# Performance work log

Hardware: AMD Instinct MI355X
Metric: run time of the kernel (lower is better)

The kernel has to match this reference:

```python
import jax, jax.numpy as jnp
import numpy as np
from jax import lax

K = 3  # kernel_size


def _leaky(x):
    return jnp.where(x >= 0, x, 0.1 * x)


def _conv3x3(x, w, b):
    # x: (B,C,H,W), w: (O,C,3,3)
    out = lax.conv_general_dilated(x, w, (1, 1), [(1, 1), (1, 1)],
                                   dimension_numbers=('NCHW', 'OIHW', 'NCHW'))
    return out + b[None, :, None, None]


def _da_conv(x, d, kw1, kw2, cw, cb, ca1, ca2):
    # per-sample dynamic depthwise conv + 1x1 conv + channel attention
    b, c, h, w = x.shape
    p = (K - 1) // 2
    # predicted per-(sample,channel) KxK kernels: (b, c*K*K) -> (b*c, 1, K, K)
    kern = (_leaky(d @ kw1.T) @ kw2.T).reshape(b * c, 1, K, K)
    out = lax.conv_general_dilated(x.reshape(1, b * c, h, w), kern, (1, 1),
                                   [(p, p), (p, p)], feature_group_count=b * c,
                                   dimension_numbers=('NCHW', 'OIHW', 'NCHW'))
    out = _leaky(out).reshape(b, c, h, w)
    # 1x1 conv with bias
    out = jnp.einsum('bchw,oc->bohw', out, cw) + cb[None, :, None, None]
    # CA layer: sigmoid(W2 @ leaky(W1 @ d)) per sample
    att = jax.nn.sigmoid(_leaky(d @ ca1.T) @ ca2.T)  # (b, c_out)
    return out + x * att[:, :, None, None]


def _forward(x, d,
             da1_kw1, da1_kw2, da1_cw, da1_cb, da1_ca1, da1_ca2,
             da2_kw1, da2_kw2, da2_cw, da2_cb, da2_ca1, da2_ca2,
             conv1_w, conv1_b, conv2_w, conv2_b, conv3_w, conv3_b,
             add_w1, add_w2):
    out = _leaky(_da_conv(x, d, da1_kw1, da1_kw2, da1_cw, da1_cb, da1_ca1, da1_ca2))
    out = _leaky(_conv3x3(out, conv1_w, conv1_b))
    # additive map: (b, 1024) -> (b,1,32,32) -> nearest-upsample to (H,W)
    add = (_leaky(d @ add_w1.T) @ add_w2.T).reshape(-1, 1, 32, 32)
    H = out.shape[-1]
    idx = jnp.arange(H) * 32 // H  # PyTorch 'nearest' index rule
    add = add[:, :, idx[:, None], idx[None, :]]
    out = out + add
    out = _conv3x3(out, conv2_w, conv2_b)
    out = _leaky(_da_conv(out, d, da2_kw1, da2_kw2, da2_cw, da2_cb, da2_ca1, da2_ca2))
    return _conv3x3(out, conv3_w, conv3_b) + x


def setup_inputs() -> dict:
    B, C, H, W = 8, 64, 192, 192
    RED = 8
    key = jax.random.key(0)
    ks = jax.random.split(key, 24)
    n = lambda k, shape, s=0.05: jax.random.normal(k, shape, jnp.float32) * s
    inp = {
        'x': jax.random.normal(ks[0], (B, C, H, W), jnp.float32),
        'd': jax.random.normal(ks[1], (B, C), jnp.float32),
    }
    for i, pfx in enumerate(['da1', 'da2']):
        base = 2 + i * 6
        inp[f'{pfx}_kw1'] = n(ks[base + 0], (64, 64))
        inp[f'{pfx}_kw2'] = n(ks[base + 1], (C * K * K, 64))
        inp[f'{pfx}_cw'] = n(ks[base + 2], (C, C))   # 1x1 conv weight (O,I)
        inp[f'{pfx}_cb'] = n(ks[base + 3], (C,))
        inp[f'{pfx}_ca1'] = n(ks[base + 4], (C // RED, 64))
        inp[f'{pfx}_ca2'] = n(ks[base + 5], (C, C // RED))
    for i, pfx in enumerate(['conv1', 'conv2', 'conv3']):
        inp[f'{pfx}_w'] = n(ks[14 + 2 * i], (C, C, K, K))
        inp[f'{pfx}_b'] = n(ks[15 + 2 * i], (C,))
    inp['add_w1'] = n(ks[20], (64, 64))
    inp['add_w2'] = n(ks[21], (32 * 32, 64))
    return inp


def reference(x, d,
              da1_kw1, da1_kw2, da1_cw, da1_cb, da1_ca1, da1_ca2,
              da2_kw1, da2_kw2, da2_cw, da2_cb, da2_ca1, da2_ca2,
              conv1_w, conv1_b, conv2_w, conv2_b, conv3_w, conv3_b,
              add_w1, add_w2):
    return _forward(x, d,
                    da1_kw1, da1_kw2, da1_cw, da1_cb, da1_ca1, da1_ca2,
                    da2_kw1, da2_kw2, da2_cw, da2_cb, da2_ca1, da2_ca2,
                    conv1_w, conv1_b, conv2_w, conv2_b, conv3_w, conv3_b,
                    add_w1, add_w2)
```

## Files before the change

kernel.cpp:

```cpp
#include <hip/hip_runtime.h>
#include <math.h>

#define B_ 8
#define C_ 64
#define H_ 192
#define W_ 192
#define HW_ (H_*W_)

typedef __attribute__((ext_vector_type(8))) short bf16x8;
typedef __attribute__((ext_vector_type(4))) float f32x4;
typedef __attribute__((ext_vector_type(4))) unsigned short u16x4;
typedef __attribute__((ext_vector_type(8))) unsigned short u16x8;
typedef __attribute__((ext_vector_type(4))) unsigned int u32x4;

__device__ __forceinline__ float lk(float v){ return v >= 0.f ? v : 0.1f*v; }
__device__ __forceinline__ float bf2f(unsigned short h){ return __uint_as_float(((unsigned)h)<<16); }
__device__ __forceinline__ unsigned short f2bf(float f){
    unsigned u = __float_as_uint(f);
    return (unsigned short)((u + 0x7fffu + ((u>>16)&1u)) >> 16);
}
__device__ __forceinline__ f32x4 mfma16(bf16x8 a, bf16x8 b, f32x4 c){
    return __builtin_amdgcn_mfma_f32_16x16x32_bf16(a, b, c, 0, 0, 0);
}

__device__ __forceinline__ void xcd_decomp(int L, int& b, int& h0, int& w0){
    b = L & 7;
    int t = L >> 3;
    h0 = (t / 12) * 16;
    w0 = (t % 12) * 16;
}

#define XS_ELEMS 22528

__global__ __launch_bounds__(256) void k_small(
    const float* __restrict__ d,
    const float* __restrict__ kw1a, const float* __restrict__ kw2a,
    const float* __restrict__ ca1a, const float* __restrict__ ca2a,
    const float* __restrict__ kw1b, const float* __restrict__ kw2b,
    const float* __restrict__ ca1b, const float* __restrict__ ca2b,
    const float* __restrict__ aw1,  const float* __restrict__ aw2,
    float* __restrict__ kern1, float* __restrict__ att1,
    float* __restrict__ kern2, float* __restrict__ att2,
    float* __restrict__ addm)
{
    int b = blockIdx.x, tid = threadIdx.x;
    __shared__ float sd[64], sv[64], su[8];
    if (tid < 64) sd[tid] = d[b*64 + tid];
    __syncthreads();
    if (tid < 64){ float s=0.f; for(int k=0;k<64;k++) s += sd[k]*kw1a[tid*64+k]; sv[tid]=lk(s); }
    if (tid >= 64 && tid < 72){ int r=tid-64; float s=0.f; for(int k=0;k<64;k++) s += sd[k]*ca1a[r*64+k]; su[r]=lk(s); }
    __syncthreads();
    for (int i=tid;i<576;i+=256){ float s=0.f; for(int j=0;j<64;j++) s += sv[j]*kw2a[i*64+j]; kern1[b*576+i]=s; }
    if (tid < 64){ float s=0.f; for(int r=0;r<8;r++) s += su[r]*ca2a[tid*8+r]; att1[b*64+tid]=1.f/(1.f+expf(-s)); }
    __syncthreads();
    if (tid < 64){ float s=0.f; for(int k=0;k<64;k++) s += sd[k]*kw1b[tid*64+k]; sv[tid]=lk(s); }
    if (tid >= 64 && tid < 72){ int r=tid-64; float s=0.f; for(int k=0;k<64;k++) s += sd[k]*ca1b[r*64+k]; su[r]=lk(s); }
    __syncthreads();
    for (int i=tid;i<576;i+=256){ float s=0.f; for(int j=0;j<64;j++) s += sv[j]*kw2b[i*64+j]; kern2[b*576+i]=s; }
    if (tid < 64){ float s=0.f; for(int r=0;r<8;r++) s += su[r]*ca2b[tid*8+r]; att2[b*64+tid]=1.f/(1.f+expf(-s)); }
    __syncthreads();
    if (tid < 64){ float s=0.f; for(int k=0;k<64;k++) s += sd[k]*aw1[tid*64+k]; sv[tid]=lk(s); }
    __syncthreads();
    for (int i=tid;i<1024;i+=256){ float s=0.f; for(int j=0;j<64;j++) s += sv[j]*aw2[i*64+j]; addm[b*1024+i]=s; }
}

__global__ __launch_bounds__(256) void k_prep(
    const float* __restrict__ w1, const float* __restrict__ w2, const float* __restrict__ w3,
    const float* __restrict__ cw1, const float* __restrict__ cw2,
    unsigned short* __restrict__ wA1, unsigned short* __restrict__ wA2, unsigned short* __restrict__ wA3,
    unsigned short* __restrict__ cwA1, unsigned short* __restrict__ cwA2,
    unsigned short* __restrict__ zp)
{
    int blk = blockIdx.x;
    if (blk < 192){
        const float* w = (blk < 64) ? w1 : (blk < 128) ? w2 : w3;
        unsigned short* wA = (blk < 64) ? wA1 : (blk < 128) ? wA2 : wA3;
        int oc = blk & 63;
        for (int i = threadIdx.x; i < 576; i += 256){
            int t = i >> 6, ic = i & 63;
            wA[oc*576 + i] = f2bf(w[oc*576 + ic*9 + t]);
        }
    } else {
        int i = (blk - 192)*256 + threadIdx.x;
        if (i < 4096) cwA1[i] = f2bf(cw1[i]);
        else          cwA2[i-4096] = f2bf(cw2[i-4096]);
        if (blk == 223 && threadIdx.x < 32) zp[threadIdx.x] = 0;
    }
}

__global__ __launch_bounds__(256) void k_xprep(const float* __restrict__ xf, unsigned short* __restrict__ xb){
    int L = blockIdx.x;
    int b = L & 7, px0 = (L >> 3)*256;
    int tid = threadIdx.x;
    __shared__ unsigned short ts[256*64];
    int q = tid >> 5, p = tid & 31;
    #pragma unroll 1
    for (int j=0; j<8; j++){
        int px = p + 32*j;
        u16x8 o;
        #pragma unroll
        for (int i=0; i<8; i++)
            o[i] = f2bf(xf[((size_t)(b*64 + q*8 + i))*HW_ + px0 + px]);
        *(u16x8*)&ts[px*64 + ((q ^ (px&7))*8)] = o;
    }
    __syncthreads();
    int k = tid & 7, pg = tid >> 3;
    #pragma unroll 1
    for (int j=0; j<8; j++){
        int px = pg + 32*j;
        u32x4 v = *(const u32x4*)&ts[px*64 + ((k ^ (px&7))*8)];
        *(u32x4*)&xb[((size_t)(b*HW_) + px0 + px)*64 + k*8] = v;
    }
}

__device__ __forceinline__ void stage_gl(const unsigned short* __restrict__ in,
                                         unsigned short* xs,
                                         const unsigned short* __restrict__ zp,
                                         int b, int h0, int w0, int wv, int lane)
{
    #pragma unroll
    for (int i=0; i<11; i++){
        int e = i*256 + wv*64 + lane;
        int pix = e >> 3;
        int j = (e & 7) ^ (pix & 7);
        int r = pix/18, col = pix - r*18;
        int gh = h0 - 1 + r, gw = w0 - 1 + col;
        const unsigned short* src = (gh >= 0 && gh < H_ && gw >= 0 && gw < W_)
            ? &in[((size_t)(b*HW_ + gh*W_ + gw))*64 + j*8] : zp;
        __builtin_amdgcn_global_load_lds(
            (const __attribute__((address_space(1))) void*)src,
            (__attribute__((address_space(3))) void*)&xs[(size_t)(i*256 + wv*64)*8],
            16, 0, 0);
    }
}

__device__ __forceinline__ void conv_main(const unsigned short* xs,
                                          const unsigned short* __restrict__ wbase,
                                          bf16x8 afr[2][2],
                                          int n, int g, int rowbase, f32x4 acc[2][8])
{
    #pragma unroll 1
    for (int t=0; t<9; t++){
        bf16x8 nxt[2][2];
        if (t < 8){
            #pragma unroll
            for (int mf=0; mf<2; mf++)
                #pragma unroll
                for (int kf=0; kf<2; kf++)
                    nxt[mf][kf] = *(const bf16x8*)(wbase + mf*(16*576) + (t+1)*64 + kf*32);
        }
        int dy = t/3, dx = t - dy*3;
        #pragma unroll
        for (int r=0; r<8; r++){
            int pix = (rowbase + r + dy)*18 + (n + dx);
            int sw = pix & 7;
            #pragma unroll
            for (int kf=0; kf<2; kf++){
                bf16x8 bfr = *(const bf16x8*)&xs[pix*64 + (((kf*4+g) ^ sw)*8)];
                acc[0][r] = mfma16(afr[0][kf], bfr, acc[0][r]);
                acc[1][r] = mfma16(afr[1][kf], bfr, acc[1][r]);
            }
        }
        if (t < 8){
            #pragma unroll
            for (int mf=0; mf<2; mf++)
                #pragma unroll
                for (int kf=0; kf<2; kf++) afr[mf][kf] = nxt[mf][kf];
        }
    }
}

template<int MODE>
__global__ __launch_bounds__(256) void k_conv(
    const unsigned short* __restrict__ in,
    const unsigned short* __restrict__ wA,
    const float* __restrict__ bias,
    const float* __restrict__ addm,
    const unsigned short* __restrict__ zp,
    unsigned short* __restrict__ outb)
{
    int b, h0, w0; xcd_decomp(blockIdx.x, b, h0, w0);
    int tid = threadIdx.x;
    __shared__ unsigned short xs[XS_ELEMS];

    int lane = tid & 63, wv = tid >> 6;
    int n = lane & 15, g = lane >> 4;
    int ochalf = (wv & 1)*32, rowbase = (wv >> 1)*8;

    stage_gl(in, xs, zp, b, h0, w0, wv, lane);

    const unsigned short* wbase = wA + (size_t)(ochalf + n)*576 + g*8;
    bf16x8 afr[2][2];
    #pragma unroll
    for (int mf=0; mf<2; mf++)
        #pragma unroll
        for (int kf=0; kf<2; kf++)
            afr[mf][kf] = *(const bf16x8*)(wbase + mf*(16*576) + kf*32);

    __syncthreads();

    f32x4 acc[2][8];
    f32x4 zz = {0.f,0.f,0.f,0.f};
    #pragma unroll
    for (int mf=0; mf<2; mf++)
        #pragma unroll
        for (int r=0; r<8; r++) acc[mf][r] = zz;

    conv_main(xs, wbase, afr, n, g, rowbase, acc);

    #pragma unroll
    for (int r=0; r<8; r++){
        int h = h0 + rowbase + r, w = w0 + n;
        float addv = 0.f;
        if (MODE == 0) addv = addm[b*1024 + (h/6)*32 + (w/6)];
        #pragma unroll
        for (int mf=0; mf<2; mf++){
            int oc0 = ochalf + mf*16 + g*4;
            f32x4 v = acc[mf][r];
            f32x4 b4 = *(const f32x4*)&bias[oc0];
            u16x4 o;
            #pragma unroll
            for (int j=0;j<4;j++){
                float val = v[j] + b4[j];
                if (MODE == 0) val = lk(val) + addv;
                o[j] = f2bf(val);
            }
            *(u16x4*)&outb[((size_t)(b*HW_ + h*W_ + w))*64 + oc0] = o;
        }
    }
}

__global__ __launch_bounds__(256) void kc3(
    const unsigned short* __restrict__ in,
    const unsigned short* __restrict__ wA,
    const float* __restrict__ bias,
    const unsigned short* __restrict__ xresb,
    const unsigned short* __restrict__ zp,
    float* __restrict__ outf)
{
    int b, h0, w0; xcd_decomp(blockIdx.x, b, h0, w0);
    int tid = threadIdx.x;
    __shared__ unsigned short xs[XS_ELEMS];

    int lane = tid & 63, wv = tid >> 6;
    int n = lane & 15, g = lane >> 4;
    int ochalf = (wv & 1)*32, rowbase = (wv >> 1)*8;

    stage_gl(in, xs, zp, b, h0, w0, wv, lane);

    const unsigned short* wbase = wA + (size_t)(ochalf + n)*576 + g*8;
    bf16x8 afr[2][2];
    #pragma unroll
    for (int mf=0; mf<2; mf++)
        #pragma unroll
        for (int kf=0; kf<2; kf++)
            afr[mf][kf] = *(const bf16x8*)(wbase + mf*(16*576) + kf*32);

    __syncthreads();

    f32x4 acc[2][8];
    f32x4 zz = {0.f,0.f,0.f,0.f};
    #pragma unroll
    for (int mf=0; mf<2; mf++)
        #pragma unroll
        for (int r=0; r<8; r++) acc[mf][r] = zz;

    conv_main(xs, wbase, afr, n, g, rowbase, acc);

    __syncthreads();
    unsigned short* ys = xs;

    #pragma unroll
    for (int mf=0; mf<2; mf++){
        int oc0 = ochalf + mf*16 + g*4;
        int sw = ((oc0 >> 2) & 3) << 2;
        f32x4 b4 = *(const f32x4*)&bias[oc0];
        #pragma unroll
        for (int r=0; r<8; r++){
            int h = h0 + rowbase + r, w = w0 + n;
            int px = (rowbase + r)*16 + n;
            u16x4 xr = *(const u16x4*)&xresb[((size_t)(b*HW_ + h*W_ + w))*64 + oc0];
            f32x4 v = acc[mf][r];
            #pragma unroll
            for (int j=0; j<4; j++)
                ys[(oc0 + j)*256 + (px ^ sw)] = f2bf(v[j] + b4[j] + bf2f(xr[j]));
        }
    }
    __syncthreads();

    int q = lane & 3, rr = lane >> 2;
    #pragma unroll 1
    for (int pass=0; pass<16; pass++){
        int oc = wv + pass*4;
        int sw = ((oc >> 2) & 3) << 2;
        int px = (rr*16 + q*4) ^ sw;
        u16x4 t = *(const u16x4*)&ys[oc*256 + px];
        size_t gidx = ((size_t)(b*C_ + oc))*HW_ + (size_t)(h0 + rr)*W_ + w0 + q*4;
        f32x4 o;
        #pragma unroll
        for (int j=0; j<4; j++) o[j] = bf2f(t[j]);
        *(f32x4*)&outf[gidx] = o;
    }
}

__device__ __forceinline__ void dw_pass(const unsigned short* xs, const float* skT,
                                        int r0, int cc, int gg, bf16x8 pbv[4])
{
    float acc[4][8];
    #pragma unroll
    for (int k=0;k<4;k++)
        #pragma unroll
        for (int i=0;i<8;i++) acc[k][i] = 0.f;

    #pragma unroll
    for (int ir=0; ir<6; ir++){
        float f[3][8];
        #pragma unroll
        for (int dx=0; dx<3; dx++){
            int spix = (r0+ir)*18 + cc + dx;
            bf16x8 v = *(const bf16x8*)&xs[spix*64 + ((gg ^ (spix&7))*8)];
            #pragma unroll
            for (int i=0;i<8;i++) f[dx][i] = bf2f((unsigned short)v[i]);
        }
        #pragma unroll
        for (int k=0;k<4;k++){
            if (ir >= k && ir <= k+2){
                int dy = ir - k;
                #pragma unroll
                for (int dx=0; dx<3; dx++){
                    f32x4 ka = *(const f32x4*)&skT[(dy*3+dx)*64 + gg*8];
                    f32x4 kb = *(const f32x4*)&skT[(dy*3+dx)*64 + gg*8 + 4];
                    #pragma unroll
                    for (int i=0;i<4;i++){
                        acc[k][i]   = fmaf(f[dx][i],   ka[i], acc[k][i]);
                        acc[k][i+4] = fmaf(f[dx][i+4], kb[i], acc[k][i+4]);
                    }
                }
            }
        }
    }
    #pragma unroll
    for (int k=0;k<4;k++){
        bf16x8 pb;
        #pragma unroll
        for (int i=0;i<8;i++) pb[i] = (short)f2bf(lk(acc[k][i]));
        pbv[k] = pb;
    }
}

__global__ __launch_bounds__(256) void k_da(
    const unsigned short* __restrict__ xb,
    const float* __restrict__ kern,
    const float* __restrict__ att,
    const unsigned short* __restrict__ cwA,
    const float* __restrict__ cb,
    const unsigned short* __restrict__ zp,
    unsigned short* __restrict__ outb)
{
    int b, h0, w0; xcd_decomp(blockIdx.x, b, h0, w0);
    int tid = threadIdx.x;
    __shared__ unsigned short xs[XS_ELEMS];
    __shared__ float skernT[576];

    int lane = tid & 63, wv = tid >> 6;
    int cc = lane & 15, g = lane >> 4;
    int r0 = wv*4;

    stage_gl(xb, xs, zp, b, h0, w0, wv, lane);

    for (int i = tid; i < 576; i += 256)
        skernT[i] = kern[b*576 + (i & 63)*9 + (i >> 6)];

    bf16x8 afr[4][2];
    #pragma unroll
    for (int mf=0; mf<4; mf++)
        #pragma unroll
        for (int kf=0; kf<2; kf++)
            afr[mf][kf] = *(const bf16x8*)&cwA[(size_t)(mf*16 + cc)*64 + kf*32 + g*8];

    __syncthreads();

    f32x4 accm[4][4];
    f32x4 zz = {0.f,0.f,0.f,0.f};
    #pragma unroll
    for (int k=0;k<4;k++)
        #pragma unroll
        for (int mf=0; mf<4; mf++) accm[k][mf] = zz;

    bf16x8 pbv[4];
    dw_pass(xs, skernT, r0, cc, g, pbv);
    #pragma unroll
    for (int k=0;k<4;k++)
        #pragma unroll
        for (int mf=0; mf<4; mf++)
            accm[k][mf] = mfma16(afr[mf][0], pbv[k], accm[k][mf]);

    dw_pass(xs, skernT, r0, cc, 4+g, pbv);
    #pragma unroll
    for (int k=0;k<4;k++)
        #pragma unroll
        for (int mf=0; mf<4; mf++)
            accm[k][mf] = mfma16(afr[mf][1], pbv[k], accm[k][mf]);

    #pragma unroll
    for (int k=0;k<4;k++){
        int r = r0 + k;
        int h = h0 + r, w = w0 + cc;
        int spix = (r+1)*18 + (cc+1);
        int sw7 = spix & 7;
        #pragma unroll
        for (int mf=0; mf<4; mf++){
            int oc0 = mf*16 + g*4;
            f32x4 v = accm[k][mf];
            f32x4 cb4 = *(const f32x4*)&cb[oc0];
            f32x4 at4 = *(const f32x4*)&att[b*64 + oc0];
            int jg = (oc0 >> 3) ^ sw7;
            u16x4 xr = *(const u16x4*)&xs[spix*64 + jg*8 + (oc0 & 7)];
            u16x4 o;
            #pragma unroll
            for (int j=0; j<4; j++){
                float val = v[j] + cb4[j] + bf2f(xr[j])*at4[j];
                o[j] = f2bf(lk(val));
            }
            *(u16x4*)&outb[((size_t)(b*HW_ + h*W_ + w))*64 + oc0] = o;
        }
    }
}

extern "C" void kernel_launch(void* const* d_in, const int* in_sizes, int n_in,
                              void* d_out, int out_size, void* d_ws, size_t ws_size,
                              hipStream_t stream)
{
    const float* x       = (const float*)d_in[0];
    const float* d       = (const float*)d_in[1];
    const float* da1_kw1 = (const float*)d_in[2];
    const float* da1_kw2 = (const float*)d_in[3];
    const float* da1_cw  = (const float*)d_in[4];
    const float* da1_cb  = (const float*)d_in[5];
    const float* da1_ca1 = (const float*)d_in[6];
    const float* da1_ca2 = (const float*)d_in[7];
    const float* da2_kw1 = (const float*)d_in[8];
    const float* da2_kw2 = (const float*)d_in[9];
    const float* da2_cw  = (const float*)d_in[10];
    const float* da2_cb  = (const float*)d_in[11];
    const float* da2_ca1 = (const float*)d_in[12];
    const float* da2_ca2 = (const float*)d_in[13];
    const float* conv1_w = (const float*)d_in[14];
    const float* conv1_b = (const float*)d_in[15];
    const float* conv2_w = (const float*)d_in[16];
    const float* conv2_b = (const float*)d_in[17];
    const float* conv3_w = (const float*)d_in[18];
    const float* conv3_b = (const float*)d_in[19];
    const float* add_w1  = (const float*)d_in[20];
    const float* add_w2  = (const float*)d_in[21];

    float* wsf   = (float*)d_ws;
    float* kern1 = wsf;
    float* att1  = wsf + 4608;
    float* kern2 = wsf + 5120;
    float* att2  = wsf + 9728;
    float* addm  = wsf + 10240;
    unsigned short* wsb  = (unsigned short*)(wsf + 18432);
    unsigned short* wA1  = wsb;
    unsigned short* wA2  = wA1 + 36864;
    unsigned short* wA3  = wA2 + 36864;
    unsigned short* cwA1 = wA3 + 36864;
    unsigned short* cwA2 = cwA1 + 4096;
    unsigned short* xbuf = cwA2 + 4096;
    const size_t N = (size_t)B_*HW_*64;
    unsigned short* buf0 = xbuf + N;
    unsigned short* buf1 = buf0 + N;
    unsigned short* zpage = buf1 + N;

    k_small<<<B_, 256, 0, stream>>>(d, da1_kw1, da1_kw2, da1_ca1, da1_ca2,
                                    da2_kw1, da2_kw2, da2_ca1, da2_ca2,
                                    add_w1, add_w2, kern1, att1, kern2, att2, addm);
    k_prep<<<224, 256, 0, stream>>>(conv1_w, conv2_w, conv3_w, da1_cw, da2_cw,
                                    wA1, wA2, wA3, cwA1, cwA2, zpage);
    k_xprep<<<1152, 256, 0, stream>>>(x, xbuf);

    k_da<<<1152, 256, 0, stream>>>(xbuf, kern1, att1, cwA1, da1_cb, zpage, buf0);
    k_conv<0><<<1152, 256, 0, stream>>>(buf0, wA1, conv1_b, addm, zpage, buf1);
    k_conv<1><<<1152, 256, 0, stream>>>(buf1, wA2, conv2_b, nullptr, zpage, buf0);
    k_da<<<1152, 256, 0, stream>>>(buf0, kern2, att2, cwA2, da2_cb, zpage, buf1);
    kc3<<<1152, 256, 0, stream>>>(buf1, wA3, conv3_b, xbuf, zpage, (float*)d_out);

    (void)in_sizes; (void)n_in; (void)out_size; (void)ws_size;
}
```

Before: 256.7 us.

## Double-buffer halo staging across three 8x16 tiles per block in conv kernels

Each of the five main conv kernels now handles three consecutive 8x16 tiles per block instead of one 16x16 tile. Async global-to-LDS loads of the next tile's halo go into a second LDS buffer while the current tile computes, synchronised with explicit vmcnt waits and barriers. The grid shrinks to 768 blocks. The goal is to hide load latency behind MFMA work. In exchange, smaller tiles re-read more halo rows, and the hand-written waitcnt and barrier sequence is fragile.

```diff
diff --git a/kernel.cpp b/kernel.cpp
--- a/kernel.cpp
+++ b/kernel.cpp
@@ -23,14 +23,6 @@
     return __builtin_amdgcn_mfma_f32_16x16x32_bf16(a, b, c, 0, 0, 0);
 }
 
-__device__ __forceinline__ void xcd_decomp(int L, int& b, int& h0, int& w0){
-    b = L & 7;
-    int t = L >> 3;
-    h0 = (t / 12) * 16;
-    w0 = (t % 12) * 16;
-}
-
-#define XS_ELEMS 22528
 
 __global__ __launch_bounds__(256) void k_small(
     const float* __restrict__ d,
@@ -113,32 +105,44 @@
     }
 }
 
-__device__ __forceinline__ void stage_gl(const unsigned short* __restrict__ in,
-                                         unsigned short* xs,
-                                         const unsigned short* __restrict__ zp,
-                                         int b, int h0, int w0, int wv, int lane)
+__device__ __forceinline__ void stage_issue(const unsigned short* __restrict__ in,
+                                            unsigned short* buf,
+                                            const unsigned short* __restrict__ zp,
+                                            int b, int h0, int w0, int wv, int lane)
 {
     #pragma unroll
-    for (int i=0; i<11; i++){
+    for (int i=0; i<6; i++){
         int e = i*256 + wv*64 + lane;
         int pix = e >> 3;
         int j = (e & 7) ^ (pix & 7);
         int r = pix/18, col = pix - r*18;
         int gh = h0 - 1 + r, gw = w0 - 1 + col;
-        const unsigned short* src = (gh >= 0 && gh < H_ && gw >= 0 && gw < W_)
+        const unsigned short* src = (pix < 180 && gh >= 0 && gh < H_ && gw >= 0 && gw < W_)
             ? &in[((size_t)(b*HW_ + gh*W_ + gw))*64 + j*8] : zp;
         __builtin_amdgcn_global_load_lds(
             (const __attribute__((address_space(1))) void*)src,
-            (__attribute__((address_space(3))) void*)&xs[(size_t)(i*256 + wv*64)*8],
+            (__attribute__((address_space(3))) void*)&buf[(size_t)(i*256 + wv*64)*8],
             16, 0, 0);
     }
 }
 
-__device__ __forceinline__ void conv_main(const unsigned short* xs,
-                                          const unsigned short* __restrict__ wbase,
-                                          bf16x8 afr[2][2],
-                                          int n, int g, int rowbase, f32x4 acc[2][8])
-{
+#define WAIT_K0()  asm volatile("s_waitcnt vmcnt(0) lgkmcnt(0)" ::: "memory")
+#define WAIT_PIPE() asm volatile("s_waitcnt vmcnt(8)" ::: "memory")
+#define BAR() __builtin_amdgcn_s_barrier()
+#define SCHED_FENCE() __builtin_amdgcn_sched_barrier(0)
+#define MEM_FENCE() asm volatile("" ::: "memory")
+
+__device__ __forceinline__ void conv_main8(const unsigned short* xs,
+                                           const unsigned short* __restrict__ wbase,
+                                           int n, int g, int rowbase, f32x4 acc[2][4])
+{
+    bf16x8 afr[2][2];
+    #pragma unroll
+    for (int mf=0; mf<2; mf++)
+        #pragma unroll
+        for (int kf=0; kf<2; kf++)
+            afr[mf][kf] = *(const bf16x8*)(wbase + mf*(16*576) + kf*32);
+
     #pragma unroll 1
     for (int t=0; t<9; t++){
         bf16x8 nxt[2][2];
@@ -151,7 +155,7 @@
         }
         int dy = t/3, dx = t - dy*3;
         #pragma unroll
-        for (int r=0; r<8; r++){
+        for (int r=0; r<4; r++){
             int pix = (rowbase + r + dy)*18 + (n + dx);
             int sw = pix & 7;
             #pragma unroll
@@ -179,54 +183,63 @@
     const unsigned short* __restrict__ zp,
     unsigned short* __restrict__ outb)
 {
-    int b, h0, w0; xcd_decomp(blockIdx.x, b, h0, w0);
+    int L = blockIdx.x;
+    int b = L & 7, s0 = (L >> 3)*3;
     int tid = threadIdx.x;
-    __shared__ unsigned short xs[XS_ELEMS];
+    __shared__ unsigned short xsd[2][12288];
 
     int lane = tid & 63, wv = tid >> 6;
     int n = lane & 15, g = lane >> 4;
-    int ochalf = (wv & 1)*32, rowbase = (wv >> 1)*8;
-
-    stage_gl(in, xs, zp, b, h0, w0, wv, lane);
-
+    int ochalf = (wv & 1)*32, rowbase = (wv >> 1)*4;
     const unsigned short* wbase = wA + (size_t)(ochalf + n)*576 + g*8;
-    bf16x8 afr[2][2];
-    #pragma unroll
-    for (int mf=0; mf<2; mf++)
-        #pragma unroll
-        for (int kf=0; kf<2; kf++)
-            afr[mf][kf] = *(const bf16x8*)(wbase + mf*(16*576) + kf*32);
-
-    __syncthreads();
-
-    f32x4 acc[2][8];
-    f32x4 zz = {0.f,0.f,0.f,0.f};
-    #pragma unroll
-    for (int mf=0; mf<2; mf++)
-        #pragma unroll
-        for (int r=0; r<8; r++) acc[mf][r] = zz;
-
-    conv_main(xs, wbase, afr, n, g, rowbase, acc);
-
-    #pragma unroll
-    for (int r=0; r<8; r++){
-        int h = h0 + rowbase + r, w = w0 + n;
-        float addv = 0.f;
-        if (MODE == 0) addv = addm[b*1024 + (h/6)*32 + (w/6)];
-        #pragma unroll
-        for (int mf=0; mf<2; mf++){
-            int oc0 = ochalf + mf*16 + g*4;
-            f32x4 v = acc[mf][r];
-            f32x4 b4 = *(const f32x4*)&bias[oc0];
-            u16x4 o;
-            #pragma unroll
-            for (int j=0;j<4;j++){
-                float val = v[j] + b4[j];
-                if (MODE == 0) val = lk(val) + addv;
-                o[j] = f2bf(val);
+
+    stage_issue(in, xsd[0], zp, b, (s0/12)*8, (s0%12)*16, wv, lane);
+
+    #pragma unroll 1
+    for (int k=0; k<3; k++){
+        int s = s0 + k;
+        int h0 = (s/12)*8, w0 = (s%12)*16;
+
+        if (k == 0) WAIT_K0(); else WAIT_PIPE();
+        BAR(); SCHED_FENCE();
+
+        if (k < 2){
+            int sn = s0 + k + 1;
+            stage_issue(in, xsd[(k+1)&1], zp, b, (sn/12)*8, (sn%12)*16, wv, lane);
+        }
+        SCHED_FENCE();
+
+        const unsigned short* xs = xsd[k&1];
+        f32x4 acc[2][4];
+        f32x4 zz = {0.f,0.f,0.f,0.f};
+        #pragma unroll
+        for (int mf=0; mf<2; mf++)
+            #pragma unroll
+            for (int r=0; r<4; r++) acc[mf][r] = zz;
+
+        conv_main8(xs, wbase, n, g, rowbase, acc);
+
+        #pragma unroll
+        for (int r=0; r<4; r++){
+            int h = h0 + rowbase + r, w = w0 + n;
+            float addv = 0.f;
+            if (MODE == 0) addv = addm[b*1024 + (h/6)*32 + (w/6)];
+            #pragma unroll
+            for (int mf=0; mf<2; mf++){
+                int oc0 = ochalf + mf*16 + g*4;
+                f32x4 v = acc[mf][r];
+                f32x4 b4 = *(const f32x4*)&bias[oc0];
+                u16x4 o;
+                #pragma unroll
+                for (int j=0;j<4;j++){
+                    float val = v[j] + b4[j];
+                    if (MODE == 0) val = lk(val) + addv;
+                    o[j] = f2bf(val);
+                }
+                *(u16x4*)&outb[((size_t)(b*HW_ + h*W_ + w))*64 + oc0] = o;
             }
-            *(u16x4*)&outb[((size_t)(b*HW_ + h*W_ + w))*64 + oc0] = o;
-        }
+        }
+        MEM_FENCE(); SCHED_FENCE(); BAR();
     }
 }
 
@@ -238,82 +251,102 @@
     const unsigned short* __restrict__ zp,
     float* __restrict__ outf)
 {
-    int b, h0, w0; xcd_decomp(blockIdx.x, b, h0, w0);
+    int L = blockIdx.x;
+    int b = L & 7, s0 = (L >> 3)*3;
     int tid = threadIdx.x;
-    __shared__ unsigned short xs[XS_ELEMS];
+    __shared__ unsigned short xsd[2][12288];
 
     int lane = tid & 63, wv = tid >> 6;
     int n = lane & 15, g = lane >> 4;
-    int ochalf = (wv & 1)*32, rowbase = (wv >> 1)*8;
-
-    stage_gl(in, xs, zp, b, h0, w0, wv, lane);
-
+    int ochalf = (wv & 1)*32, rowbase = (wv >> 1)*4;
     const unsigned short* wbase = wA + (size_t)(ochalf + n)*576 + g*8;
-    bf16x8 afr[2][2];
+
+    stage_issue(in, xsd[0], zp, b, (s0/12)*8, (s0%12)*16, wv, lane);
+
+    #pragma unroll 1
+    for (int k=0; k<3; k++){
+        int s = s0 + k;
+        int h0 = (s/12)*8, w0 = (s%12)*16;
+
+        if (k == 0) WAIT_K0(); else WAIT_PIPE();
+        BAR(); SCHED_FENCE();
+
+        if (k < 2){
+            int sn = s0 + k + 1;
+            stage_issue(in, xsd[(k+1)&1], zp, b, (sn/12)*8, (sn%12)*16, wv, lane);
+        }
+        SCHED_FENCE();
+
+        unsigned short* xs = xsd[k&1];
+        f32x4 acc[2][4];
+        f32x4 zz = {0.f,0.f,0.f,0.f};
+        #pragma unroll
+        for (int mf=0; mf<2; mf++)
+            #pragma unroll
+            for (int r=0; r<4; r++) acc[mf][r] = zz;
+
+        conv_main8(xs, wbase, n, g, rowbase, acc);
+
+        u16x4 xr[2][4];
+        #pragma unroll
+        for (int mf=0; mf<2; mf++){
+            int oc0 = ochalf + mf*16 + g*4;
+            #pragma unroll
+            for (int r=0; r<4; r++){
+                int h = h0 + rowbase + r, w = w0 + n;
+                xr[mf][r] = *(const u16x4*)&xresb[((size_t)(b*HW_ + h*W_ + w))*64 + oc0];
+            }
+        }
+
+        asm volatile("s_waitcnt lgkmcnt(0)" ::: "memory");
+        BAR();
+        unsigned short* ys = xs;
+
+        #pragma unroll
+        for (int mf=0; mf<2; mf++){
+            int oc0 = ochalf + mf*16 + g*4;
+            int sw = ((oc0 >> 2) & 3) << 2;
+            f32x4 b4 = *(const f32x4*)&bias[oc0];
+            #pragma unroll
+            for (int r=0; r<4; r++){
+                int px = (rowbase + r)*16 + n;
+                f32x4 v = acc[mf][r];
+                #pragma unroll
+                for (int j=0; j<4; j++)
+                    ys[(oc0 + j)*128 + (px ^ sw)] = f2bf(v[j] + b4[j] + bf2f(xr[mf][r][j]));
+            }
+        }
+        asm volatile("s_waitcnt lgkmcnt(0)" ::: "memory");
+        BAR();
+
+        int q = lane & 3, rr = (lane >> 2) & 7, tt = lane >> 5;
+        #pragma unroll 1
+        for (int pass=0; pass<8; pass++){
+            int oc = pass*8 + wv*2 + tt;
+            int sw = ((oc >> 2) & 3) << 2;
+            int px = (rr*16 + q*4) ^ sw;
+            u16x4 tv = *(const u16x4*)&ys[oc*128 + px];
+            size_t gidx = ((size_t)(b*C_ + oc))*HW_ + (size_t)(h0 + rr)*W_ + w0 + q*4;
+            f32x4 o;
+            #pragma unroll
+            for (int j=0; j<4; j++) o[j] = bf2f(tv[j]);
+            *(f32x4*)&outf[gidx] = o;
+        }
+        MEM_FENCE(); SCHED_FENCE(); BAR();
+    }
+}
+
+__device__ __forceinline__ void dw_pass2(const unsigned short* xs, const float* skT,
+                                         int r0, int cc, int gg, bf16x8 pbv[2])
+{
+    float acc[2][8];
     #pragma unroll
-    for (int mf=0; mf<2; mf++)
-        #pragma unroll
-        for (int kf=0; kf<2; kf++)
-            afr[mf][kf] = *(const bf16x8*)(wbase + mf*(16*576) + kf*32);
-
-    __syncthreads();
-
-    f32x4 acc[2][8];
-    f32x4 zz = {0.f,0.f,0.f,0.f};
+    for (int k=0;k<2;k++)
+        #pragma unroll
+        for (int i=0;i<8;i++) acc[k][i] = 0.f;
+
     #pragma unroll
-    for (int mf=0; mf<2; mf++)
-        #pragma unroll
-        for (int r=0; r<8; r++) acc[mf][r] = zz;
-
-    conv_main(xs, wbase, afr, n, g, rowbase, acc);
-
-    __syncthreads();
-    unsigned short* ys = xs;
-
-    #pragma unroll
-    for (int mf=0; mf<2; mf++){
-        int oc0 = ochalf + mf*16 + g*4;
-        int sw = ((oc0 >> 2) & 3) << 2;
-        f32x4 b4 = *(const f32x4*)&bias[oc0];
-        #pragma unroll
-        for (int r=0; r<8; r++){
-            int h = h0 + rowbase + r, w = w0 + n;
-            int px = (rowbase + r)*16 + n;
-            u16x4 xr = *(const u16x4*)&xresb[((size_t)(b*HW_ + h*W_ + w))*64 + oc0];
-            f32x4 v = acc[mf][r];
-            #pragma unroll
-            for (int j=0; j<4; j++)
-                ys[(oc0 + j)*256 + (px ^ sw)] = f2bf(v[j] + b4[j] + bf2f(xr[j]));
-        }
-    }
-    __syncthreads();
-
-    int q = lane & 3, rr = lane >> 2;
-    #pragma unroll 1
-    for (int pass=0; pass<16; pass++){
-        int oc = wv + pass*4;
-        int sw = ((oc >> 2) & 3) << 2;
-        int px = (rr*16 + q*4) ^ sw;
-        u16x4 t = *(const u16x4*)&ys[oc*256 + px];
-        size_t gidx = ((size_t)(b*C_ + oc))*HW_ + (size_t)(h0 + rr)*W_ + w0 + q*4;
-        f32x4 o;
-        #pragma unroll
-        for (int j=0; j<4; j++) o[j] = bf2f(t[j]);
-        *(f32x4*)&outf[gidx] = o;
-    }
-}
-
-__device__ __forceinline__ void dw_pass(const unsigned short* xs, const float* skT,
-                                        int r0, int cc, int gg, bf16x8 pbv[4])
-{
-    float acc[4][8];
-    #pragma unroll
-    for (int k=0;k<4;k++)
-        #pragma unroll
-        for (int i=0;i<8;i++) acc[k][i] = 0.f;
-
-    #pragma unroll
-    for (int ir=0; ir<6; ir++){
+    for (int ir=0; ir<4; ir++){
         float f[3][8];
         #pragma unroll
         for (int dx=0; dx<3; dx++){
@@ -323,7 +356,7 @@
             for (int i=0;i<8;i++) f[dx][i] = bf2f((unsigned short)v[i]);
         }
         #pragma unroll
-        for (int k=0;k<4;k++){
+        for (int k=0;k<2;k++){
             if (ir >= k && ir <= k+2){
                 int dy = ir - k;
                 #pragma unroll
@@ -340,7 +373,7 @@
         }
     }
     #pragma unroll
-    for (int k=0;k<4;k++){
+    for (int k=0;k<2;k++){
         bf16x8 pb;
         #pragma unroll
         for (int i=0;i<8;i++) pb[i] = (short)f2bf(lk(acc[k][i]));
@@ -357,16 +390,15 @@
     const unsigned short* __restrict__ zp,
     unsigned short* __restrict__ outb)
 {
-    int b, h0, w0; xcd_decomp(blockIdx.x, b, h0, w0);
+    int L = blockIdx.x;
+    int b = L & 7, s0 = (L >> 3)*3;
     int tid = threadIdx.x;
-    __shared__ unsigned short xs[XS_ELEMS];
+    __shared__ unsigned short xsd[2][12288];
     __shared__ float skernT[576];
 
     int lane = tid & 63, wv = tid >> 6;
     int cc = lane & 15, g = lane >> 4;
-    int r0 = wv*4;
-
-    stage_gl(xb, xs, zp, b, h0, w0, wv, lane);
+    int r0 = wv*2;
 
     for (int i = tid; i < 576; i += 256)
         skernT[i] = kern[b*576 + (i & 63)*9 + (i >> 6)];
@@ -378,52 +410,70 @@
         for (int kf=0; kf<2; kf++)
             afr[mf][kf] = *(const bf16x8*)&cwA[(size_t)(mf*16 + cc)*64 + kf*32 + g*8];
 
-    __syncthreads();
-
-    f32x4 accm[4][4];
-    f32x4 zz = {0.f,0.f,0.f,0.f};
-    #pragma unroll
-    for (int k=0;k<4;k++)
-        #pragma unroll
-        for (int mf=0; mf<4; mf++) accm[k][mf] = zz;
-
-    bf16x8 pbv[4];
-    dw_pass(xs, skernT, r0, cc, g, pbv);
-    #pragma unroll
-    for (int k=0;k<4;k++)
-        #pragma unroll
-        for (int mf=0; mf<4; mf++)
-            accm[k][mf] = mfma16(afr[mf][0], pbv[k], accm[k][mf]);
-
-    dw_pass(xs, skernT, r0, cc, 4+g, pbv);
-    #pragma unroll
-    for (int k=0;k<4;k++)
-        #pragma unroll
-        for (int mf=0; mf<4; mf++)
-            accm[k][mf] = mfma16(afr[mf][1], pbv[k], accm[k][mf]);
-
-    #pragma unroll
-    for (int k=0;k<4;k++){
-        int r = r0 + k;
-        int h = h0 + r, w = w0 + cc;
-        int spix = (r+1)*18 + (cc+1);
-        int sw7 = spix & 7;
-        #pragma unroll
-        for (int mf=0; mf<4; mf++){
-            int oc0 = mf*16 + g*4;
-            f32x4 v = accm[k][mf];
-            f32x4 cb4 = *(const f32x4*)&cb[oc0];
-            f32x4 at4 = *(const f32x4*)&att[b*64 + oc0];
-            int jg = (oc0 >> 3) ^ sw7;
-            u16x4 xr = *(const u16x4*)&xs[spix*64 + jg*8 + (oc0 & 7)];
-            u16x4 o;
-            #pragma unroll
-            for (int j=0; j<4; j++){
-                float val = v[j] + cb4[j] + bf2f(xr[j])*at4[j];
-                o[j] = f2bf(lk(val));
+    stage_issue(xb, xsd[0], zp, b, (s0/12)*8, (s0%12)*16, wv, lane);
+
+    #pragma unroll 1
+    for (int k=0; k<3; k++){
+        int s = s0 + k;
+        int h0 = (s/12)*8, w0 = (s%12)*16;
+
+        if (k == 0) WAIT_K0(); else WAIT_PIPE();
+        BAR(); SCHED_FENCE();
+
+        if (k < 2){
+            int sn = s0 + k + 1;
+            stage_issue(xb, xsd[(k+1)&1], zp, b, (sn/12)*8, (sn%12)*16, wv, lane);
+        }
+        SCHED_FENCE();
+
+        const unsigned short* xs = xsd[k&1];
+
+        f32x4 accm[2][4];
+        f32x4 zz = {0.f,0.f,0.f,0.f};
+        #pragma unroll
+        for (int it=0;it<2;it++)
+            #pragma unroll
+            for (int mf=0; mf<4; mf++) accm[it][mf] = zz;
+
+        bf16x8 pbv[2];
+        dw_pass2(xs, skernT, r0, cc, g, pbv);
+        #pragma unroll
+        for (int it=0;it<2;it++)
+            #pragma unroll
+            for (int mf=0; mf<4; mf++)
+                accm[it][mf] = mfma16(afr[mf][0], pbv[it], accm[it][mf]);
+
+        dw_pass2(xs, skernT, r0, cc, 4+g, pbv);
+        #pragma unroll
+        for (int it=0;it<2;it++)
+            #pragma unroll
+            for (int mf=0; mf<4; mf++)
+                accm[it][mf] = mfma16(afr[mf][1], pbv[it], accm[it][mf]);
+
+        #pragma unroll
+        for (int it=0;it<2;it++){
+            int r = r0 + it;
+            int h = h0 + r, w = w0 + cc;
+            int spix = (r+1)*18 + (cc+1);
+            int sw7 = spix & 7;
+            #pragma unroll
+            for (int mf=0; mf<4; mf++){
+                int oc0 = mf*16 + g*4;
+                f32x4 v = accm[it][mf];
+                f32x4 cb4 = *(const f32x4*)&cb[oc0];
+                f32x4 at4 = *(const f32x4*)&att[b*64 + oc0];
+                int jg = (oc0 >> 3) ^ sw7;
+                u16x4 xr = *(const u16x4*)&xs[spix*64 + jg*8 + (oc0 & 7)];
+                u16x4 o;
+                #pragma unroll
+                for (int j=0; j<4; j++){
+                    float val = v[j] + cb4[j] + bf2f(xr[j])*at4[j];
+                    o[j] = f2bf(lk(val));
+                }
+                *(u16x4*)&outb[((size_t)(b*HW_ + h*W_ + w))*64 + oc0] = o;
             }
-            *(u16x4*)&outb[((size_t)(b*HW_ + h*W_ + w))*64 + oc0] = o;
-        }
+        }
+        MEM_FENCE(); SCHED_FENCE(); BAR();
     }
 }
 
@@ -479,11 +529,11 @@
                                     wA1, wA2, wA3, cwA1, cwA2, zpage);
     k_xprep<<<1152, 256, 0, stream>>>(x, xbuf);
 
-    k_da<<<1152, 256, 0, stream>>>(xbuf, kern1, att1, cwA1, da1_cb, zpage, buf0);
-    k_conv<0><<<1152, 256, 0, stream>>>(buf0, wA1, conv1_b, addm, zpage, buf1);
-    k_conv<1><<<1152, 256, 0, stream>>>(buf1, wA2, conv2_b, nullptr, zpage, buf0);
-    k_da<<<1152, 256, 0, stream>>>(buf0, kern2, att2, cwA2, da2_cb, zpage, buf1);
-    kc3<<<1152, 256, 0, stream>>>(buf1, wA3, conv3_b, xbuf, zpage, (float*)d_out);
+    k_da<<<768, 256, 0, stream>>>(xbuf, kern1, att1, cwA1, da1_cb, zpage, buf0);
+    k_conv<0><<<768, 256, 0, stream>>>(buf0, wA1, conv1_b, addm, zpage, buf1);
+    k_conv<1><<<768, 256, 0, stream>>>(buf1, wA2, conv2_b, nullptr, zpage, buf0);
+    k_da<<<768, 256, 0, stream>>>(buf0, kern2, att2, cwA2, da2_cb, zpage, buf1);
+    kc3<<<768, 256, 0, stream>>>(buf1, wA3, conv3_b, xbuf, zpage, (float*)d_out);
 
     (void)in_sizes; (void)n_in; (void)out_size; (void)ws_size;
 }
```

Result: slower. 268.6 us (+4.7%).

## Double threads per tile in conv and DA kernels, halving rows per wave

Applied to the files above, without the earlier changes.

The four tile kernels now launch 512 threads instead of 256. Each wave handles half as many output rows (4 instead of 8 in the convs, 2 instead of 4 in the depthwise path), and the halo staging loop and LDS buffer are resized to cover 512 threads, with out-of-range pixels redirected to the zero page. The aim is more waves in flight to hide LDS and global latency and lower per-thread register pressure. The cost is less reuse of the weight fragments per wave and more redundant halo row reads in the depthwise pass.

```diff
diff --git a/kernel.cpp b/kernel.cpp
--- a/kernel.cpp
+++ b/kernel.cpp
@@ -30,7 +30,7 @@
     w0 = (t % 12) * 16;
 }
 
-#define XS_ELEMS 22528
+#define XS_ELEMS 24576
 
 __global__ __launch_bounds__(256) void k_small(
     const float* __restrict__ d,
@@ -119,25 +119,25 @@
                                          int b, int h0, int w0, int wv, int lane)
 {
     #pragma unroll
-    for (int i=0; i<11; i++){
-        int e = i*256 + wv*64 + lane;
+    for (int i=0; i<6; i++){
+        int e = i*512 + wv*64 + lane;
         int pix = e >> 3;
         int j = (e & 7) ^ (pix & 7);
         int r = pix/18, col = pix - r*18;
         int gh = h0 - 1 + r, gw = w0 - 1 + col;
-        const unsigned short* src = (gh >= 0 && gh < H_ && gw >= 0 && gw < W_)
+        const unsigned short* src = (pix < 324 && gh >= 0 && gh < H_ && gw >= 0 && gw < W_)
             ? &in[((size_t)(b*HW_ + gh*W_ + gw))*64 + j*8] : zp;
         __builtin_amdgcn_global_load_lds(
             (const __attribute__((address_space(1))) void*)src,
-            (__attribute__((address_space(3))) void*)&xs[(size_t)(i*256 + wv*64)*8],
+            (__attribute__((address_space(3))) void*)&xs[(size_t)(i*512 + wv*64)*8],
             16, 0, 0);
     }
 }
 
-__device__ __forceinline__ void conv_main(const unsigned short* xs,
-                                          const unsigned short* __restrict__ wbase,
-                                          bf16x8 afr[2][2],
-                                          int n, int g, int rowbase, f32x4 acc[2][8])
+__device__ __forceinline__ void conv_main4(const unsigned short* xs,
+                                           const unsigned short* __restrict__ wbase,
+                                           bf16x8 afr[2][2],
+                                           int n, int g, int rowbase, f32x4 acc[2][4])
 {
     #pragma unroll 1
     for (int t=0; t<9; t++){
@@ -151,7 +151,7 @@
         }
         int dy = t/3, dx = t - dy*3;
         #pragma unroll
-        for (int r=0; r<8; r++){
+        for (int r=0; r<4; r++){
             int pix = (rowbase + r + dy)*18 + (n + dx);
             int sw = pix & 7;
             #pragma unroll
@@ -171,7 +171,7 @@
 }
 
 template<int MODE>
-__global__ __launch_bounds__(256) void k_conv(
+__global__ __launch_bounds__(512) void k_conv(
     const unsigned short* __restrict__ in,
     const unsigned short* __restrict__ wA,
     const float* __restrict__ bias,
@@ -185,7 +185,7 @@
 
     int lane = tid & 63, wv = tid >> 6;
     int n = lane & 15, g = lane >> 4;
-    int ochalf = (wv & 1)*32, rowbase = (wv >> 1)*8;
+    int ochalf = (wv & 1)*32, rowbase = (wv >> 1)*4;
 
     stage_gl(in, xs, zp, b, h0, w0, wv, lane);
 
@@ -199,17 +199,17 @@
 
     __syncthreads();
 
-    f32x4 acc[2][8];
+    f32x4 acc[2][4];
     f32x4 zz = {0.f,0.f,0.f,0.f};
     #pragma unroll
     for (int mf=0; mf<2; mf++)
         #pragma unroll
-        for (int r=0; r<8; r++) acc[mf][r] = zz;
-
-    conv_main(xs, wbase, afr, n, g, rowbase, acc);
-
-    #pragma unroll
-    for (int r=0; r<8; r++){
+        for (int r=0; r<4; r++) acc[mf][r] = zz;
+
+    conv_main4(xs, wbase, afr, n, g, rowbase, acc);
+
+    #pragma unroll
+    for (int r=0; r<4; r++){
         int h = h0 + rowbase + r, w = w0 + n;
         float addv = 0.f;
         if (MODE == 0) addv = addm[b*1024 + (h/6)*32 + (w/6)];
@@ -230,7 +230,7 @@
     }
 }
 
-__global__ __launch_bounds__(256) void kc3(
+__global__ __launch_bounds__(512) void kc3(
     const unsigned short* __restrict__ in,
     const unsigned short* __restrict__ wA,
     const float* __restrict__ bias,
@@ -244,7 +244,7 @@
 
     int lane = tid & 63, wv = tid >> 6;
     int n = lane & 15, g = lane >> 4;
-    int ochalf = (wv & 1)*32, rowbase = (wv >> 1)*8;
+    int ochalf = (wv & 1)*32, rowbase = (wv >> 1)*4;
 
     stage_gl(in, xs, zp, b, h0, w0, wv, lane);
 
@@ -258,14 +258,14 @@
 
     __syncthreads();
 
-    f32x4 acc[2][8];
+    f32x4 acc[2][4];
     f32x4 zz = {0.f,0.f,0.f,0.f};
     #pragma unroll
     for (int mf=0; mf<2; mf++)
         #pragma unroll
-        for (int r=0; r<8; r++) acc[mf][r] = zz;
-
-    conv_main(xs, wbase, afr, n, g, rowbase, acc);
+        for (int r=0; r<4; r++) acc[mf][r] = zz;
+
+    conv_main4(xs, wbase, afr, n, g, rowbase, acc);
 
     __syncthreads();
     unsigned short* ys = xs;
@@ -276,7 +276,7 @@
         int sw = ((oc0 >> 2) & 3) << 2;
         f32x4 b4 = *(const f32x4*)&bias[oc0];
         #pragma unroll
-        for (int r=0; r<8; r++){
+        for (int r=0; r<4; r++){
             int h = h0 + rowbase + r, w = w0 + n;
             int px = (rowbase + r)*16 + n;
             u16x4 xr = *(const u16x4*)&xresb[((size_t)(b*HW_ + h*W_ + w))*64 + oc0];
@@ -290,8 +290,8 @@
 
     int q = lane & 3, rr = lane >> 2;
     #pragma unroll 1
-    for (int pass=0; pass<16; pass++){
-        int oc = wv + pass*4;
+    for (int pass=0; pass<8; pass++){
+        int oc = wv + pass*8;
         int sw = ((oc >> 2) & 3) << 2;
         int px = (rr*16 + q*4) ^ sw;
         u16x4 t = *(const u16x4*)&ys[oc*256 + px];
@@ -303,17 +303,17 @@
     }
 }
 
-__device__ __forceinline__ void dw_pass(const unsigned short* xs, const float* skT,
-                                        int r0, int cc, int gg, bf16x8 pbv[4])
-{
-    float acc[4][8];
-    #pragma unroll
-    for (int k=0;k<4;k++)
+__device__ __forceinline__ void dw_pass2(const unsigned short* xs, const float* skT,
+                                         int r0, int cc, int gg, bf16x8 pbv[2])
+{
+    float acc[2][8];
+    #pragma unroll
+    for (int k=0;k<2;k++)
         #pragma unroll
         for (int i=0;i<8;i++) acc[k][i] = 0.f;
 
     #pragma unroll
-    for (int ir=0; ir<6; ir++){
+    for (int ir=0; ir<4; ir++){
         float f[3][8];
         #pragma unroll
         for (int dx=0; dx<3; dx++){
@@ -323,7 +323,7 @@
             for (int i=0;i<8;i++) f[dx][i] = bf2f((unsigned short)v[i]);
         }
         #pragma unroll
-        for (int k=0;k<4;k++){
+        for (int k=0;k<2;k++){
             if (ir >= k && ir <= k+2){
                 int dy = ir - k;
                 #pragma unroll
@@ -340,7 +340,7 @@
         }
     }
     #pragma unroll
-    for (int k=0;k<4;k++){
+    for (int k=0;k<2;k++){
         bf16x8 pb;
         #pragma unroll
         for (int i=0;i<8;i++) pb[i] = (short)f2bf(lk(acc[k][i]));
@@ -348,7 +348,7 @@
     }
 }
 
-__global__ __launch_bounds__(256) void k_da(
+__global__ __launch_bounds__(512) void k_da(
     const unsigned short* __restrict__ xb,
     const float* __restrict__ kern,
     const float* __restrict__ att,
@@ -364,11 +364,11 @@
 
     int lane = tid & 63, wv = tid >> 6;
     int cc = lane & 15, g = lane >> 4;
-    int r0 = wv*4;
+    int r0 = wv*2;
 
     stage_gl(xb, xs, zp, b, h0, w0, wv, lane);
 
-    for (int i = tid; i < 576; i += 256)
+    for (int i = tid; i < 576; i += 512)
         skernT[i] = kern[b*576 + (i & 63)*9 + (i >> 6)];
 
     bf16x8 afr[4][2];
@@ -380,38 +380,38 @@
 
     __syncthreads();
 
-    f32x4 accm[4][4];
+    f32x4 accm[2][4];
     f32x4 zz = {0.f,0.f,0.f,0.f};
     #pragma unroll
-    for (int k=0;k<4;k++)
-        #pragma unroll
-        for (int mf=0; mf<4; mf++) accm[k][mf] = zz;
-
-    bf16x8 pbv[4];
-    dw_pass(xs, skernT, r0, cc, g, pbv);
-    #pragma unroll
-    for (int k=0;k<4;k++)
+    for (int it=0;it<2;it++)
+        #pragma unroll
+        for (int mf=0; mf<4; mf++) accm[it][mf] = zz;
+
+    bf16x8 pbv[2];
+    dw_pass2(xs, skernT, r0, cc, g, pbv);
+    #pragma unroll
+    for (int it=0;it<2;it++)
         #pragma unroll
         for (int mf=0; mf<4; mf++)
-            accm[k][mf] = mfma16(afr[mf][0], pbv[k], accm[k][mf]);
-
-    dw_pass(xs, skernT, r0, cc, 4+g, pbv);
-    #pragma unroll
-    for (int k=0;k<4;k++)
+            accm[it][mf] = mfma16(afr[mf][0], pbv[it], accm[it][mf]);
+
+    dw_pass2(xs, skernT, r0, cc, 4+g, pbv);
+    #pragma unroll
+    for (int it=0;it<2;it++)
         #pragma unroll
         for (int mf=0; mf<4; mf++)
-            accm[k][mf] = mfma16(afr[mf][1], pbv[k], accm[k][mf]);
-
-    #pragma unroll
-    for (int k=0;k<4;k++){
-        int r = r0 + k;
+            accm[it][mf] = mfma16(afr[mf][1], pbv[it], accm[it][mf]);
+
+    #pragma unroll
+    for (int it=0;it<2;it++){
+        int r = r0 + it;
         int h = h0 + r, w = w0 + cc;
         int spix = (r+1)*18 + (cc+1);
         int sw7 = spix & 7;
         #pragma unroll
         for (int mf=0; mf<4; mf++){
             int oc0 = mf*16 + g*4;
-            f32x4 v = accm[k][mf];
+            f32x4 v = accm[it][mf];
             f32x4 cb4 = *(const f32x4*)&cb[oc0];
             f32x4 at4 = *(const f32x4*)&att[b*64 + oc0];
             int jg = (oc0 >> 3) ^ sw7;
@@ -479,11 +479,11 @@
                                     wA1, wA2, wA3, cwA1, cwA2, zpage);
     k_xprep<<<1152, 256, 0, stream>>>(x, xbuf);
 
-    k_da<<<1152, 256, 0, stream>>>(xbuf, kern1, att1, cwA1, da1_cb, zpage, buf0);
-    k_conv<0><<<1152, 256, 0, stream>>>(buf0, wA1, conv1_b, addm, zpage, buf1);
-    k_conv<1><<<1152, 256, 0, stream>>>(buf1, wA2, conv2_b, nullptr, zpage, buf0);
-    k_da<<<1152, 256, 0, stream>>>(buf0, kern2, att2, cwA2, da2_cb, zpage, buf1);
-    kc3<<<1152, 256, 0, stream>>>(buf1, wA3, conv3_b, xbuf, zpage, (float*)d_out);
+    k_da<<<1152, 512, 0, stream>>>(xbuf, kern1, att1, cwA1, da1_cb, zpage, buf0);
+    k_conv<0><<<1152, 512, 0, stream>>>(buf0, wA1, conv1_b, addm, zpage, buf1);
+    k_conv<1><<<1152, 512, 0, stream>>>(buf1, wA2, conv2_b, nullptr, zpage, buf0);
+    k_da<<<1152, 512, 0, stream>>>(buf0, kern2, att2, cwA2, da2_cb, zpage, buf1);
+    kc3<<<1152, 512, 0, stream>>>(buf1, wA3, conv3_b, xbuf, zpage, (float*)d_out);
 
     (void)in_sizes; (void)n_in; (void)out_size; (void)ws_size;
 }
```

Result: slower. 288.5 us (+12.4%).
